# Optimization experiments

Hardware: AMD Instinct MI355X
Metric: run time of the kernel (lower is better)

Reference implementation:

```python
import jax, jax.numpy as jnp
import numpy as np

N, B, C, K, H = 65536, 4, 512, 256, 8


def setup_inputs() -> dict:
    key = jax.random.key(0)
    ks = jax.random.split(key, 6)
    feat = jax.random.normal(ks[0], (N, C), dtype=jnp.float32)
    cls_tokens = jax.random.normal(ks[1], (B, C), dtype=jnp.float32)
    Wqkv = jax.random.normal(ks[2], (C, 3 * C), dtype=jnp.float32) * 0.02
    bqkv = jnp.zeros((3 * C,), dtype=jnp.float32)
    Wproj = jax.random.normal(ks[3], (C, C), dtype=jnp.float32) * 0.02
    bproj = jnp.zeros((C,), dtype=jnp.float32)
    order = jax.random.permutation(ks[4], N)          # serialized order (permutation)
    inverse = jnp.argsort(order)                       # its inverse
    offset = jnp.arange(1, B + 1) * (N // B)           # equal-size point clouds, divisible by K
    return {"feat": feat, "cls_tokens": cls_tokens, "Wqkv": Wqkv, "bqkv": bqkv,
            "Wproj": Wproj, "bproj": bproj, "order": order, "inverse": inverse,
            "offset": offset, "patch_size": K, "num_heads": H}


def reference(feat, cls_tokens, Wqkv, bqkv, Wproj, bproj, order, inverse, offset, patch_size, num_heads):
    n, c = feat.shape
    b = offset.shape[0]
    k = patch_size
    h = num_heads
    dh = c // h
    scale = dh ** -0.5
    n_chunks = n // k

    # qkv projection, gather into serialized order
    qkv = (feat @ Wqkv + bqkv)[order]                  # [N, 3C]
    cls_qkv = cls_tokens @ Wqkv + bqkv                 # [B, 3C]

    # chunk -> batch assignment (offsets are chunk-aligned here)
    chunk_starts = jnp.arange(n_chunks) * k
    batch_id = jnp.searchsorted(offset, chunk_starts, side="right")  # [n_chunks]
    acc = jax.nn.one_hot(batch_id, b, dtype=feat.dtype)              # [n_chunks, B]
    agg = acc.T / acc.T.sum(axis=1, keepdims=True)                   # [B, n_chunks]

    cls_per_chunk = acc @ cls_qkv                                    # [n_chunks, 3C]
    qkv_c = qkv.reshape(n_chunks, k, 3 * c)
    qkv_c = jnp.concatenate([cls_per_chunk[:, None, :], qkv_c], axis=1)  # [n_chunks, K+1, 3C]

    qkv_c = qkv_c.reshape(n_chunks, k + 1, 3, h, dh)
    q = qkv_c[:, :, 0].transpose(0, 2, 1, 3)           # [n_chunks, H, K+1, dh]
    kk = qkv_c[:, :, 1].transpose(0, 2, 1, 3)
    v = qkv_c[:, :, 2].transpose(0, 2, 1, 3)

    # upcast_attention / upcast_softmax = True
    attn = jnp.einsum("nhqd,nhkd->nhqk", q.astype(jnp.float32) * scale, kk.astype(jnp.float32))
    attn = jax.nn.softmax(attn, axis=-1).astype(feat.dtype)
    out = jnp.einsum("nhqk,nhkd->nhqd", attn, v)       # [n_chunks, H, K+1, dh]
    out = out.transpose(0, 2, 1, 3).reshape(n_chunks, k + 1, c)

    feat_out = out[:, 1:, :].reshape(-1, c)[inverse]   # scatter back to original order
    feat_out = feat_out @ Wproj + bproj                # proj (proj_drop is identity in eval)
    cls_feat = agg @ out[:, 0, :]                      # [B, C] (no proj, per source)
    return feat_out, cls_feat
```

## Files before the change

kernel.cpp:

```cpp
#include <hip/hip_runtime.h>


typedef float  floatx4 __attribute__((ext_vector_type(4)));
typedef __bf16 bf16x8  __attribute__((ext_vector_type(8)));

__device__ __forceinline__ __bf16 f2bf(float x) {
  unsigned u = __builtin_bit_cast(unsigned, x);
  u = u + 0x7FFFu + ((u >> 16) & 1u);
  unsigned short h = (unsigned short)(u >> 16);
  return __builtin_bit_cast(__bf16, h);
}

__device__ __forceinline__ floatx4 mfma_16x16x32(bf16x8 a, bf16x8 b, floatx4 c) {
  return __builtin_amdgcn_mfma_f32_16x16x32_bf16(a, b, c, 0, 0, 0);
}

__device__ __forceinline__ void gload16(const void* g, void* l) {
  __builtin_amdgcn_global_load_lds(
      (const __attribute__((address_space(1))) unsigned int*)g,
      (__attribute__((address_space(3))) unsigned int*)l, 16, 0, 0);
}

__global__ void cast_gather_feat(const float* __restrict__ feat,
                                 const int* __restrict__ order,
                                 __bf16* __restrict__ dst) {
  long i = ((long)blockIdx.x * blockDim.x + threadIdx.x) * 8;
  int row = (int)(i >> 9);
  int col = (int)(i & 511);
  const float* sp = feat + (long)order[row] * 512 + col;
  float4 a = *(const float4*)sp;
  float4 b = *(const float4*)(sp + 4);
  bf16x8 o;
  o[0] = f2bf(a.x); o[1] = f2bf(a.y); o[2] = f2bf(a.z); o[3] = f2bf(a.w);
  o[4] = f2bf(b.x); o[5] = f2bf(b.y); o[6] = f2bf(b.z); o[7] = f2bf(b.w);
  *(bf16x8*)(dst + i) = o;
}

__global__ void transpose_cast(const float* __restrict__ W, __bf16* __restrict__ Wt,
                               int K, int N) {
  __shared__ float tile[32][33];
  const int n0 = blockIdx.x * 32, k0 = blockIdx.y * 32;
  const int c = threadIdx.x & 31, r8 = threadIdx.x >> 5;
#pragma unroll
  for (int i = 0; i < 4; ++i) {
    int r = r8 + i * 8;
    tile[r][c] = W[(long)(k0 + r) * N + n0 + c];
  }
  __syncthreads();
#pragma unroll
  for (int i = 0; i < 4; ++i) {
    int r = r8 + i * 8;
    Wt[(long)(n0 + r) * K + k0 + c] = f2bf(tile[c][r]);
  }
}

__global__ void cls_qkv_kernel(const float* __restrict__ cls_tokens,
                               const float* __restrict__ Wqkv,
                               const float* __restrict__ bqkv,
                               __bf16* __restrict__ clsqkv, int N3) {
  __shared__ float red[256];
  const int c = threadIdx.x & 63, part = threadIdx.x >> 6;
  const int o = blockIdx.x * 64 + c;
  const int b = o / N3, n = o - b * N3;
  float sv = 0.f;
  const int kst = part * 128;
  for (int k = kst; k < kst + 128; ++k)
    sv += cls_tokens[b * 512 + k] * Wqkv[(long)k * N3 + n];
  red[threadIdx.x] = sv;
  __syncthreads();
  if (part == 0)
    clsqkv[o] = f2bf(red[c] + red[c + 64] + red[c + 128] + red[c + 192] + bqkv[n]);
}

template <int OUT_F32, int COLS>
__global__ __launch_bounds__(256, 2) void gemm_bt(
    const __bf16* __restrict__ A, const __bf16* __restrict__ Bt,
    const float* __restrict__ bias, void* __restrict__ C,
    int N, int K) {
  __shared__ __align__(16) __bf16 As[128 * 64];
  __shared__ __align__(16) __bf16 Bs[128 * 64];
  const int tid = threadIdx.x;
  const int wave = tid >> 6, lane = tid & 63;
  const int quad = lane >> 4, l15 = lane & 15;
  const int wr = wave >> 1, wc = wave & 1;
  const int per = gridDim.x >> 3;
  const int work = (blockIdx.x & 7) * per + (blockIdx.x >> 3);
  const int rowblk = work / COLS, colblk = work - rowblk * COLS;
  const long m0 = (long)rowblk * 128;
  const int n0 = colblk * 128;
  const int srow8 = lane >> 3;
  const int sc8p = lane & 7;

  floatx4 zero = {0.f, 0.f, 0.f, 0.f};
  floatx4 acc[4][4];
#pragma unroll
  for (int i = 0; i < 4; ++i)
#pragma unroll
    for (int j = 0; j < 4; ++j) acc[i][j] = zero;

  for (int kt = 0; kt < K; kt += 64) {
    __syncthreads();
#pragma unroll
    for (int i = 0; i < 4; ++i) {
      const int rbase = i * 32 + wave * 8;
      const int row = rbase + srow8;
      const int c8 = sc8p ^ (row & 7);
      gload16(A + (m0 + row) * K + kt + c8 * 8, As + rbase * 64);
      gload16(Bt + (long)(n0 + row) * K + kt + c8 * 8, Bs + rbase * 64);
    }
    __syncthreads();
#pragma unroll
    for (int ks = 0; ks < 2; ++ks) {
      bf16x8 af[4], bfr[4];
#pragma unroll
      for (int mi = 0; mi < 4; ++mi) {
        int row = wr * 64 + mi * 16 + l15;
        int c8 = ks * 4 + quad;
        af[mi] = *(const bf16x8*)(As + row * 64 + ((c8 ^ (row & 7)) << 3));
      }
#pragma unroll
      for (int ni = 0; ni < 4; ++ni) {
        int row = wc * 64 + ni * 16 + l15;
        int c8 = ks * 4 + quad;
        bfr[ni] = *(const bf16x8*)(Bs + row * 64 + ((c8 ^ (row & 7)) << 3));
      }
#pragma unroll
      for (int mi = 0; mi < 4; ++mi)
#pragma unroll
        for (int ni = 0; ni < 4; ++ni)
          acc[mi][ni] = mfma_16x16x32(af[mi], bfr[ni], acc[mi][ni]);
    }
  }
#pragma unroll
  for (int mi = 0; mi < 4; ++mi) {
#pragma unroll
    for (int ni = 0; ni < 4; ++ni) {
      const int col = n0 + wc * 64 + ni * 16 + l15;
      const float bb = bias[col];
#pragma unroll
      for (int r = 0; r < 4; ++r) {
        const long row = m0 + wr * 64 + mi * 16 + quad * 4 + r;
        float v = acc[mi][ni][r] + bb;
        if (OUT_F32)
          ((float*)C)[row * N + col] = v;
        else
          ((__bf16*)C)[row * N + col] = f2bf(v);
      }
    }
  }
}

__global__ __launch_bounds__(256, 2) void attn_kernel(
    const __bf16* __restrict__ qkv,
    const __bf16* __restrict__ clsqkv,
    const int* __restrict__ order,
    const int* __restrict__ offset,
    __bf16* __restrict__ outO,
    float* __restrict__ outcls,
    int B) {
  __shared__ __align__(16) __bf16 Ks[272 * 64];
  __shared__ __align__(16) __bf16 Vt[64 * 264 + 64];
  __shared__ __align__(16) __bf16 Pbuf[4 * 16 * 40];
  const int chunk = blockIdx.x & 255;
  const int h = blockIdx.x >> 8;
  const int tid = threadIdx.x;
  const int wave = tid >> 6, lane = tid & 63;
  const int quad = lane >> 4, l15 = lane & 15;
  const int cs = chunk << 8;
  int batch = 0;
  for (int b = 0; b < B; ++b) batch += (offset[b] <= cs) ? 1 : 0;
  const unsigned clsoff =
      (unsigned)((const char*)(clsqkv + (long)batch * 1536) - (const char*)qkv);

  const int qoffB = h * 128;
  const int koffB = 1024 + h * 128;
  const int voffB = 2048 + h * 128;

  auto rowoff = [&](int t) -> unsigned {
    int tt = (t <= 256) ? t : 256;
    return (tt == 0) ? clsoff : (unsigned)(cs + tt - 1) * 3072u;
  };

  {
    const int rsub = lane >> 3, c8 = lane & 7;
    for (int i = wave; i < 34; i += 4) {
      int r = i * 8 + rsub;
      gload16((const char*)qkv + rowoff(r) + koffB + ((c8 ^ (r & 7)) << 4),
              Ks + i * 512);
    }
  }

  {
    const int rsub = lane >> 3, c8 = lane & 7;
#pragma unroll
    for (int p = 0; p < 8; ++p) {
      int t = p * 32 + wave * 8 + rsub;
      unsigned ro = (t == 0) ? clsoff : (unsigned)(cs + t - 1) * 3072u;
      bf16x8 v = *(const bf16x8*)((const char*)qkv + ro + voffB + c8 * 16);
#pragma unroll
      for (int j = 0; j < 8; ++j)
        Vt[(c8 * 8 + j) * 264 + c8 * 8 + t] = v[j];
    }
    if (tid < 8) {
      bf16x8 v = *(const bf16x8*)((const char*)qkv +
                                  (unsigned)(cs + 255) * 3072u + voffB + tid * 16);
#pragma unroll
      for (int j = 0; j < 8; ++j)
        Vt[(tid * 8 + j) * 264 + tid * 8 + 256] = v[j];
    }
  }
  __syncthreads();

  int vbase[4];
#pragma unroll
  for (int ni = 0; ni < 4; ++ni) {
    int d = ni * 16 + l15;
    vbase[ni] = d * 264 + ((ni * 2 + (l15 >> 3)) & 7) * 8;
  }
  float v256[4];
#pragma unroll
  for (int ni = 0; ni < 4; ++ni) v256[ni] = (float)Vt[vbase[ni] + 256];
  __bf16* Pw = Pbuf + wave * (16 * 40);
  const int sw = l15 & 7;
  const __bf16* kb = Ks + l15 * 64;

  for (int rt = wave; rt < 17; rt += 4) {
    const unsigned qo = rowoff(rt * 16 + l15);
    bf16x8 qf0 = *(const bf16x8*)((const char*)qkv + qo + qoffB + quad * 16);
    bf16x8 qf1 = *(const bf16x8*)((const char*)qkv + qo + qoffB + 64 + quad * 16);

    floatx4 zero = {0.f, 0.f, 0.f, 0.f};
    floatx4 s[17];
#pragma unroll
    for (int i = 0; i < 17; ++i) s[i] = zero;
#pragma unroll
    for (int k2 = 0; k2 < 17; ++k2) {
      const __bf16* kr = kb + k2 * 1024;
      bf16x8 kf0 = *(const bf16x8*)(kr + ((quad ^ sw) << 3));
      bf16x8 kf1 = *(const bf16x8*)(kr + (((quad + 4) ^ sw) << 3));
      s[k2] = mfma_16x16x32(qf0, kf0, s[k2]);
      s[k2] = mfma_16x16x32(qf1, kf1, s[k2]);
    }

    float mx[4] = {-3.0e38f, -3.0e38f, -3.0e38f, -3.0e38f};
#pragma unroll
    for (int k2 = 0; k2 < 16; ++k2)
#pragma unroll
      for (int r = 0; r < 4; ++r) mx[r] = fmaxf(mx[r], s[k2][r]);
#pragma unroll
    for (int r = 0; r < 4; ++r) {
      float v = (l15 == 0) ? s[16][r] : -3.0e38f;
      s[16][r] = v;
      mx[r] = fmaxf(mx[r], v);
    }
#pragma unroll
    for (int off = 1; off < 16; off <<= 1)
#pragma unroll
      for (int r = 0; r < 4; ++r) mx[r] = fmaxf(mx[r], __shfl_xor(mx[r], off, 16));
    const float c1 = 0.125f * 1.44269504f;
    float mb[4], sum[4] = {0.f, 0.f, 0.f, 0.f};
#pragma unroll
    for (int r = 0; r < 4; ++r) mb[r] = mx[r] * c1;
#pragma unroll
    for (int k2 = 0; k2 < 17; ++k2)
#pragma unroll
      for (int r = 0; r < 4; ++r) {
        float e = __builtin_amdgcn_exp2f(fmaf(s[k2][r], c1, -mb[r]));
        s[k2][r] = e;
        sum[r] += e;
      }
#pragma unroll
    for (int off = 1; off < 16; off <<= 1)
#pragma unroll
      for (int r = 0; r < 4; ++r) sum[r] += __shfl_xor(sum[r], off, 16);
    float rl[4];
#pragma unroll
    for (int r = 0; r < 4; ++r) rl[r] = 1.0f / sum[r];

    floatx4 o[4];
#pragma unroll
    for (int i = 0; i < 4; ++i) o[i] = zero;
#pragma unroll
    for (int ks = 0; ks < 8; ++ks) {
#pragma unroll
      for (int half = 0; half < 2; ++half) {
        int kt2 = ks * 2 + half;
#pragma unroll
        for (int r = 0; r < 4; ++r)
          Pw[(quad * 4 + r) * 40 + half * 16 + l15] = f2bf(s[kt2][r]);
      }
      asm volatile("s_waitcnt lgkmcnt(0)" ::: "memory");
      bf16x8 pf = *(const bf16x8*)(Pw + l15 * 40 + quad * 8);
#pragma unroll
      for (int ni = 0; ni < 4; ++ni) {
        bf16x8 vf = *(const bf16x8*)(Vt + vbase[ni] + ks * 32 + quad * 8);
        o[ni] = mfma_16x16x32(pf, vf, o[ni]);
      }
    }
    float p256[4];
#pragma unroll
    for (int r = 0; r < 4; ++r) p256[r] = __shfl(s[16][r], lane & 48, 64);
#pragma unroll
    for (int ni = 0; ni < 4; ++ni)
#pragma unroll
      for (int r = 0; r < 4; ++r)
        o[ni][r] = (o[ni][r] + p256[r] * v256[ni]) * rl[r];

#pragma unroll
    for (int r = 0; r < 4; ++r) {
      int q = rt * 16 + quad * 4 + r;
      if (q > 256) continue;
      if (q == 0) {
#pragma unroll
        for (int ni = 0; ni < 4; ++ni)
          outcls[(long)chunk * 512 + h * 64 + ni * 16 + l15] = o[ni][r];
      } else {
        long orow = (long)order[cs + q - 1];
#pragma unroll
        for (int ni = 0; ni < 4; ++ni)
          outO[orow * 512 + h * 64 + ni * 16 + l15] = f2bf(o[ni][r]);
      }
    }
  }
}

__global__ void cls_feat_kernel(const float* __restrict__ outcls,
                                const int* __restrict__ offset,
                                float* __restrict__ dst, int B, int C) {
  int i = blockIdx.x * blockDim.x + threadIdx.x;
  if (i >= B * C) return;
  int b = i / C, c = i - b * C;
  int st = (b == 0) ? 0 : offset[b - 1];
  int en = offset[b];
  int c0 = st >> 8, c1 = en >> 8;
  float s = 0.f;
  for (int ch = c0; ch < c1; ++ch) s += outcls[(long)ch * C + c];
  dst[i] = s / (float)(c1 - c0);
}

extern "C" void kernel_launch(void* const* d_in, const int* in_sizes, int n_in,
                              void* d_out, int out_size, void* d_ws, size_t ws_size,
                              hipStream_t stream) {
  const float* feat       = (const float*)d_in[0];
  const float* cls_tokens = (const float*)d_in[1];
  const float* Wqkv       = (const float*)d_in[2];
  const float* bqkv       = (const float*)d_in[3];
  const float* Wproj      = (const float*)d_in[4];
  const float* bproj      = (const float*)d_in[5];
  const int*   order      = (const int*)d_in[6];
  const int*   offset     = (const int*)d_in[8];
  const int B = in_sizes[8];

  char* ws = (char*)d_ws;
  __bf16* qkv    = (__bf16*)(ws);
  __bf16* featb  = (__bf16*)(ws + 201326592);
  __bf16* outO   = featb;
  __bf16* wqkvT  = (__bf16*)(ws + 268435456);
  __bf16* wprojT = (__bf16*)(ws + 270008320);
  __bf16* clsqkv = (__bf16*)(ws + 270532608);
  float*  outcls = (float*)(ws + 270544896);

  float* feat_out = (float*)d_out;
  float* cls_out  = feat_out + (long)65536 * 512;

  cast_gather_feat<<<16384, 256, 0, stream>>>(feat, order, featb);
  transpose_cast<<<dim3(48, 16), 256, 0, stream>>>(Wqkv, wqkvT, 512, 1536);
  transpose_cast<<<dim3(16, 16), 256, 0, stream>>>(Wproj, wprojT, 512, 512);
  cls_qkv_kernel<<<96, 256, 0, stream>>>(cls_tokens, Wqkv, bqkv, clsqkv, 1536);

  gemm_bt<0, 12><<<6144, 256, 0, stream>>>(featb, wqkvT, bqkv, (void*)qkv, 1536, 512);

  attn_kernel<<<2048, 256, 0, stream>>>(qkv, clsqkv, order, offset, outO, outcls, B);

  gemm_bt<1, 4><<<2048, 256, 0, stream>>>(outO, wprojT, bproj, (void*)feat_out, 512, 512);

  cls_feat_kernel<<<8, 256, 0, stream>>>(outcls, offset, cls_out, B, 512);
}
```

Before: 592.4 us.

## Replace QKV GEMM with 256x256-tile eight-wave ping-pong pipelined kernel

Adds a new QKV projection GEMM that uses 256x256 output tiles with 512 threads and double-buffered LDS. Each K-step is split into four quadrant phases, and global-to-LDS loads for the next tile are interleaved with MFMA compute through explicit waitcnt, barrier and setprio scheduling. The goal is higher arithmetic intensity per tile and hiding load latency behind compute. In exchange it uses 128KB of LDS per block, which limits occupancy, and it carries hand-tuned vmcnt values that must match the load counts exactly.

Measured after the change: 623.6 us. 1.05x slower.

```diff
diff --git a/kernel.cpp b/kernel.cpp
--- a/kernel.cpp
+++ b/kernel.cpp
@@ -70,6 +70,132 @@
   __syncthreads();
   if (part == 0)
     clsqkv[o] = f2bf(red[c] + red[c + 64] + red[c + 128] + red[c + 192] + bqkv[n]);
+}
+
+#define PHASE_COMPUTE(BUF, QA, QB)                                            \
+  do {                                                                        \
+    bf16x8 af[4][2], bfr[2][2];                                               \
+    _Pragma("unroll") for (int mi = 0; mi < 4; ++mi) {                        \
+      const int row = (QA) * 128 + wm2 * 64 + mi * 16 + l15;                  \
+      _Pragma("unroll") for (int ks = 0; ks < 2; ++ks) {                      \
+        const int c8 = ks * 4 + quad;                                         \
+        af[mi][ks] =                                                          \
+            *(const bf16x8*)(&As[BUF][row * 64 + ((c8 ^ (row & 7)) << 3)]);   \
+      }                                                                       \
+    }                                                                         \
+    _Pragma("unroll") for (int ni = 0; ni < 2; ++ni) {                        \
+      const int row = (QB) * 128 + wn2 * 32 + ni * 16 + l15;                  \
+      _Pragma("unroll") for (int ks = 0; ks < 2; ++ks) {                      \
+        const int c8 = ks * 4 + quad;                                         \
+        bfr[ni][ks] =                                                         \
+            *(const bf16x8*)(&Bs[BUF][row * 64 + ((c8 ^ (row & 7)) << 3)]);   \
+      }                                                                       \
+    }                                                                         \
+    __builtin_amdgcn_s_setprio(1);                                            \
+    _Pragma("unroll") for (int mi = 0; mi < 4; ++mi)                          \
+        _Pragma("unroll") for (int ni = 0; ni < 2; ++ni)                      \
+            _Pragma("unroll") for (int ks = 0; ks < 2; ++ks)                  \
+                acc[(QA) * 4 + mi][(QB) * 2 + ni] = mfma_16x16x32(            \
+                    af[mi][ks], bfr[ni][ks], acc[(QA) * 4 + mi][(QB) * 2 + ni]); \
+    __builtin_amdgcn_s_setprio(0);                                            \
+  } while (0)
+
+#define PHASE_SYNC(VMC)                                        \
+  do {                                                         \
+    asm volatile("s_waitcnt vmcnt(" #VMC ")" ::: "memory");    \
+    __builtin_amdgcn_s_barrier();                              \
+    __builtin_amdgcn_sched_barrier(0);                         \
+  } while (0)
+
+__global__ __launch_bounds__(512, 2) void gemm_qkv_8p(
+    const __bf16* __restrict__ A,
+    const __bf16* __restrict__ Bt,
+    const float* __restrict__ bias,
+    __bf16* __restrict__ C, int N, int K) {
+  __shared__ __align__(16) __bf16 As[2][256 * 64];
+  __shared__ __align__(16) __bf16 Bs[2][256 * 64];
+  const int tid = threadIdx.x;
+  const int wave = tid >> 6, lane = tid & 63;
+  const int quad = lane >> 4, l15 = lane & 15;
+  const int wm2 = wave >> 2, wn2 = wave & 3;
+  const int per = gridDim.x >> 3;
+  const int work = (blockIdx.x & 7) * per + (blockIdx.x >> 3);
+  const int rowblk = work / 6, colblk = work - rowblk * 6;
+  const long m0 = (long)rowblk * 256;
+  const int n0 = colblk * 256;
+  const int srow8 = lane >> 3, sc8p = lane & 7;
+  const int NT = K / 64;
+
+  auto stageA = [&](int b, int rh, int t) {
+#pragma unroll
+    for (int j = 0; j < 2; ++j) {
+      const int rbase = rh * 128 + j * 64 + wave * 8;
+      const int row = rbase + srow8;
+      const int c8 = sc8p ^ (row & 7);
+      gload16(A + (m0 + row) * K + t * 64 + c8 * 8, &As[b][rbase * 64]);
+    }
+  };
+  auto stageB = [&](int b, int rh, int t) {
+#pragma unroll
+    for (int j = 0; j < 2; ++j) {
+      const int rbase = rh * 128 + j * 64 + wave * 8;
+      const int row = rbase + srow8;
+      const int c8 = sc8p ^ (row & 7);
+      gload16(Bt + (long)(n0 + row) * K + t * 64 + c8 * 8, &Bs[b][rbase * 64]);
+    }
+  };
+
+  floatx4 acc[8][4];
+#pragma unroll
+  for (int i = 0; i < 8; ++i)
+#pragma unroll
+    for (int j = 0; j < 4; ++j) acc[i][j] = floatx4{0.f, 0.f, 0.f, 0.f};
+
+  stageA(0, 0, 0); stageB(0, 0, 0); stageB(0, 1, 0); stageA(0, 1, 0);
+
+  for (int t = 0; t < NT - 1; ++t) {
+    const int cur = t & 1, nxt = cur ^ 1;
+    PHASE_SYNC(4);
+    stageA(nxt, 0, t + 1);
+    PHASE_COMPUTE(cur, 0, 0);
+    PHASE_SYNC(4);
+    stageB(nxt, 0, t + 1);
+    PHASE_COMPUTE(cur, 0, 1);
+    PHASE_SYNC(4);
+    stageB(nxt, 1, t + 1);
+    PHASE_COMPUTE(cur, 1, 0);
+    __builtin_amdgcn_s_barrier();
+    __builtin_amdgcn_sched_barrier(0);
+    stageA(nxt, 1, t + 1);
+    PHASE_COMPUTE(cur, 1, 1);
+  }
+  {
+    const int cur = (NT - 1) & 1;
+    PHASE_SYNC(4);
+    PHASE_COMPUTE(cur, 0, 0);
+    PHASE_SYNC(2);
+    PHASE_COMPUTE(cur, 0, 1);
+    PHASE_SYNC(0);
+    PHASE_COMPUTE(cur, 1, 0);
+    __builtin_amdgcn_s_barrier();
+    __builtin_amdgcn_sched_barrier(0);
+    PHASE_COMPUTE(cur, 1, 1);
+  }
+
+#pragma unroll
+  for (int mg = 0; mg < 8; ++mg) {
+#pragma unroll
+    for (int ng = 0; ng < 4; ++ng) {
+      const int col = n0 + (ng >> 1) * 128 + wn2 * 32 + (ng & 1) * 16 + l15;
+      const float bb = bias[col];
+#pragma unroll
+      for (int r = 0; r < 4; ++r) {
+        const long row =
+            m0 + (mg >> 2) * 128 + wm2 * 64 + (mg & 3) * 16 + quad * 4 + r;
+        C[row * N + col] = f2bf(acc[mg][ng][r] + bb);
+      }
+    }
+  }
 }
 
 template <int OUT_F32, int COLS>
@@ -368,7 +494,7 @@
   transpose_cast<<<dim3(16, 16), 256, 0, stream>>>(Wproj, wprojT, 512, 512);
   cls_qkv_kernel<<<96, 256, 0, stream>>>(cls_tokens, Wqkv, bqkv, clsqkv, 1536);
 
-  gemm_bt<0, 12><<<6144, 256, 0, stream>>>(featb, wqkvT, bqkv, (void*)qkv, 1536, 512);
+  gemm_qkv_8p<<<1536, 512, 0, stream>>>(featb, wqkvT, bqkv, qkv, 1536, 512);
 
   attn_kernel<<<2048, 256, 0, stream>>>(qkv, clsqkv, order, offset, outO, outcls, B);
 
```
